# Kernel tuning notes

Hardware: AMD Instinct MI355X
Metric: run time of the kernel (lower is better)

## Reference

```python
import jax, jax.numpy as jnp
import numpy as np


def mish(x):
    return x * jnp.tanh(jax.nn.softplus(x))


def gcn(x, W, b, src, dst):
    # PyG GCNConv: h = D^-1/2 (A+I) D^-1/2 (x W) + b, aggregation at dst=edge_index[1]
    n = x.shape[0]
    h = x @ W
    deg = jax.ops.segment_sum(jnp.ones(src.shape[0], x.dtype), dst, num_segments=n) + 1.0
    dinv = jax.lax.rsqrt(deg)
    msg = h[src] * (dinv[src] * dinv[dst])[:, None]
    agg = jax.ops.segment_sum(msg, dst, num_segments=n)
    return agg + h * (dinv * dinv)[:, None] + b


def pool_mean(x, seg, num_segments):
    s = jax.ops.segment_sum(x, seg, num_segments=num_segments)
    c = jax.ops.segment_sum(jnp.ones(x.shape[0], x.dtype), seg, num_segments=num_segments)
    return s / jnp.maximum(c, 1.0)[:, None]


def attention(x, qW, qb, kW, kb, vW, vb, G):
    # x: [G*R, in_feats] -> per-graph self-attention over ROIs (dropout is identity in eval)
    R = x.shape[0] // G
    xc = x.reshape(G, R, x.shape[1])
    Q = xc @ qW + qb
    K = xc @ kW + kb
    Vv = xc @ vW + vb
    scores = jnp.einsum('gqd,gkd->gqk', Q, K) / (Q.shape[-1] ** 0.5)
    w = jax.nn.softmax(scores, axis=-1)
    out = jnp.einsum('gqk,gkd->gqd', w, Vv).reshape(G * R, Vv.shape[-1])
    return out, w.mean(axis=0)


def closs(a, b, temp=0.6):
    a = a / jnp.maximum(jnp.linalg.norm(a, axis=1, keepdims=True), 1e-12)
    b = b / jnp.maximum(jnp.linalg.norm(b, axis=1, keepdims=True), 1e-12)
    logits = (a @ b.T) / temp
    return -jnp.mean(jnp.diagonal(jax.nn.log_softmax(logits, axis=1)))


def setup_inputs() -> dict:
    key = jax.random.key(0)
    G, R1, R2, F_IN, H, OUT, DEG, V = 512, 200, 160, 128, 64, 64, 16, 64
    N1, N2 = G * R1, G * R2
    ks = iter(jax.random.split(key, 64))
    d = {}
    d['x1'] = jax.random.normal(next(ks), (N1, R1 + 3), jnp.float32)
    d['x2'] = jax.random.normal(next(ks), (N2, R2 + 3), jnp.float32)

    def lin(name, i, o):
        d[name + '_W'] = jax.random.normal(next(ks), (i, o), jnp.float32) * (i ** -0.5)
        d[name + '_b'] = jnp.zeros((o,), jnp.float32)

    lin('fcl', R1 + 3, F_IN); lin('fcr', R2 + 3, F_IN)
    lin('fcl1', R1, F_IN); lin('fcr1', R2, F_IN)
    lin('a1_q', F_IN, OUT); lin('a1_k', F_IN, OUT); lin('a1_v', F_IN, OUT)
    lin('a2_q', F_IN, OUT); lin('a2_k', F_IN, OUT); lin('a2_v', F_IN, OUT)
    lin('conv', F_IN, H); lin('conv1', H, H)
    lin('mlp', H, OUT)
    lin('fc1a', OUT * 4, F_IN); lin('fc1b', F_IN, 2)

    def edges(k, R):
        k1, k2 = jax.random.split(k)
        off = (jnp.arange(G, dtype=jnp.int32) * R)[:, None]
        src = jax.random.randint(k1, (G, R * DEG), 0, R, jnp.int32) + off
        dst = jax.random.randint(k2, (G, R * DEG), 0, R, jnp.int32) + off
        return jnp.stack([src.reshape(-1), dst.reshape(-1)])

    d['edge_index1'] = edges(next(ks), R1)
    d['edge_index2'] = edges(next(ks), R2)
    d['batch1'] = jnp.repeat(jnp.arange(G, dtype=jnp.int32), R1)
    d['batch2'] = jnp.repeat(jnp.arange(G, dtype=jnp.int32), R2)

    def sub(k, R):
        # one visited-node set (as in RW_subgraph) tiled per graph with offsets
        vis = jnp.sort(jax.random.permutation(k, R)[:V]).astype(jnp.int32)
        return (vis[None, :] + (jnp.arange(G, dtype=jnp.int32) * R)[:, None]).reshape(-1)

    d['sub_idx1'] = sub(next(ks), R1)
    d['sub_idx2'] = sub(next(ks), R2)
    d['num_graphs'] = G
    return d


def reference(x1, x2, fcl_W, fcl_b, fcr_W, fcr_b, fcl1_W, fcl1_b, fcr1_W, fcr1_b,
              a1_q_W, a1_q_b, a1_k_W, a1_k_b, a1_v_W, a1_v_b,
              a2_q_W, a2_q_b, a2_k_W, a2_k_b, a2_v_W, a2_v_b,
              conv_W, conv_b, conv1_W, conv1_b, mlp_W, mlp_b,
              fc1a_W, fc1a_b, fc1b_W, fc1b_b,
              edge_index1, edge_index2, batch1, batch2, sub_idx1, sub_idx2, num_graphs):
    G = int(num_graphs)
    src1, dst1 = edge_index1[0], edge_index1[1]
    src2, dst2 = edge_index2[0], edge_index2[1]

    z1 = x1[:, :-3] @ fcl1_W + fcl1_b
    z2 = x2[:, :-3] @ fcr1_W + fcr1_b
    z1, aw1 = attention(z1, a1_q_W, a1_q_b, a1_k_W, a1_k_b, a1_v_W, a1_v_b, G)
    z2, aw2 = attention(z2, a2_q_W, a2_q_b, a2_k_W, a2_k_b, a2_v_W, a2_v_b, G)
    z1 = pool_mean(z1, batch1, G)
    z2 = pool_mean(z2, batch2, G)

    h1 = x1 @ fcl_W + fcl_b
    h2 = x2 @ fcr_W + fcr_b
    o1 = mish(gcn(h1, conv_W, conv_b, src1, dst1))
    o2 = mish(gcn(h2, conv_W, conv_b, src2, dst2))
    o1 = gcn(o1, conv1_W, conv1_b, src1, dst1)
    o2 = gcn(o2, conv1_W, conv1_b, src2, dst2)

    s1 = o1[sub_idx1] @ mlp_W + mlp_b
    s2 = o2[sub_idx2] @ mlp_W + mlp_b
    s1 = pool_mean(s1, batch1[sub_idx1], G)
    s2 = pool_mean(s2, batch2[sub_idx2], G)

    c_loss = closs(s1, z2) + closs(z1, s2)
    feat = jnp.concatenate([s1, z1, s2, z2], axis=1)
    out = mish(feat @ fc1a_W + fc1a_b) @ fc1b_W + fc1b_b
    return c_loss, out, aw1, aw2
```

## Files before the change

kernel.cpp:

```cpp
#include <hip/hip_runtime.h>
#include <math.h>

#define TPB 256
#define MAXEP 4608

typedef float f32x4 __attribute__((ext_vector_type(4)));
typedef __bf16 bfv8 __attribute__((ext_vector_type(8)));

union U8 { uint4 q; unsigned short us[8]; __bf16 b[8]; bfv8 v; };

__device__ __forceinline__ unsigned short f2bfu(float f) {
  union { __bf16 h; unsigned short u; } x;
  x.h = (__bf16)f;
  return x.u;
}
__device__ __forceinline__ float bfu2f(unsigned short u) {
  return __uint_as_float((unsigned)u << 16);
}

__device__ __forceinline__ float mish_f(float x) {
  float sp = fmaxf(x, 0.f) + log1pf(expf(-fabsf(x)));
  return x * tanhf(sp);
}

__device__ __forceinline__ U8 loadA_f32(const float* Af, int kb, int K, bool rowok) {
  U8 u;
  if (rowok && kb + 8 <= K) {
    float4 f0 = *(const float4*)(Af + kb);
    float4 f1 = *(const float4*)(Af + kb + 4);
    u.b[0]=(__bf16)f0.x; u.b[1]=(__bf16)f0.y; u.b[2]=(__bf16)f0.z; u.b[3]=(__bf16)f0.w;
    u.b[4]=(__bf16)f1.x; u.b[5]=(__bf16)f1.y; u.b[6]=(__bf16)f1.z; u.b[7]=(__bf16)f1.w;
  } else {
#pragma unroll
    for (int j = 0; j < 8; ++j) {
      float f = (rowok && kb + j < K) ? Af[kb + j] : 0.f;
      u.b[j] = (__bf16)f;
    }
  }
  return u;
}

template<bool ABF16, bool CBF16, bool MISH, int NJ, int KPMAX>
__global__ __launch_bounds__(256) void gemm2(
    const void* __restrict__ Av, const unsigned short* __restrict__ Bt,
    const float* __restrict__ bias, void* __restrict__ Cv,
    int N, int M, int K, int lda, int ldc,
    long sA, long sB, long sC, float alpha, int Kpad)
{
  constexpr int BM = NJ * 16;
  __shared__ unsigned short Bs[BM * KPMAX];

  const int tid = threadIdx.x;
  const int col0 = blockIdx.x * BM, row0 = blockIdx.y * 64;

  {
    const unsigned short* Bp = Bt + (long)blockIdx.z * sB + (long)col0 * Kpad;
    int rows = M - col0; if (rows > BM) rows = BM;
    const int total = rows * Kpad;
    for (int i = tid * 8; i < total; i += TPB * 32) {
      uint4 a0, a1, a2, a3;
      bool b1 = i + TPB * 8  < total;
      bool b2 = i + TPB * 16 < total;
      bool b3 = i + TPB * 24 < total;
      a0 = *(const uint4*)&Bp[i];
      if (b1) a1 = *(const uint4*)&Bp[i + TPB * 8];
      if (b2) a2 = *(const uint4*)&Bp[i + TPB * 16];
      if (b3) a3 = *(const uint4*)&Bp[i + TPB * 24];
      *(uint4*)&Bs[i] = a0;
      if (b1) *(uint4*)&Bs[i + TPB * 8]  = a1;
      if (b2) *(uint4*)&Bs[i + TPB * 16] = a2;
      if (b3) *(uint4*)&Bs[i + TPB * 24] = a3;
    }
  }

  const int lane = tid & 63, w = tid >> 6;
  const int mrow = lane & 15, kg = lane >> 4;
  const int arow = row0 + w * 16 + mrow;
  const bool rowok = arow < N;

  const unsigned short* Ah = nullptr;
  const float* Af = nullptr;
  if (ABF16) Ah = (const unsigned short*)Av + (long)blockIdx.z * sA + (long)arow * lda;
  else       Af = (const float*)Av + (long)blockIdx.z * sA + (long)arow * lda;

  U8 ua;
  if (ABF16) ua.q = *(const uint4*)(Ah + kg * 8);
  else       ua   = loadA_f32(Af, kg * 8, K, rowok);

  __syncthreads();

  f32x4 acc[NJ];
#pragma unroll
  for (int j = 0; j < NJ; ++j) acc[j] = (f32x4)0.f;

  for (int k0 = 0; k0 < K; k0 += 32) {
    U8 un;
    bool more = (k0 + 32) < K;
    if (more) {
      if (ABF16) un.q = *(const uint4*)(Ah + k0 + 32 + kg * 8);
      else       un   = loadA_f32(Af, k0 + 32 + kg * 8, K, rowok);
    }
    const int kb = k0 + kg * 8;
#pragma unroll
    for (int j = 0; j < NJ; ++j) {
      U8 ub;
      ub.q = *(const uint4*)&Bs[(j * 16 + mrow) * Kpad + kb];
      acc[j] = __builtin_amdgcn_mfma_f32_16x16x32_bf16(ua.v, ub.v, acc[j], 0, 0, 0);
    }
    if (more) ua = un;
  }

  long cbase = (long)blockIdx.z * sC;
#pragma unroll
  for (int j = 0; j < NJ; ++j) {
    int gc = col0 + j * 16 + mrow;
    if (gc >= M) continue;
    float bb = bias ? bias[gc] : 0.f;
#pragma unroll
    for (int r = 0; r < 4; ++r) {
      int gr = row0 + w * 16 + kg * 4 + r;
      if (gr >= N) continue;
      float v = acc[j][r] * alpha + bb;
      if (MISH) v = mish_f(v);
      if (CBF16) ((unsigned short*)Cv)[cbase + (long)gr * ldc + gc] = f2bfu(v);
      else       ((float*)Cv)[cbase + (long)gr * ldc + gc] = v;
    }
  }
}

static inline int kpad_of(int K) { return ((K + 31) / 32) * 32 + 8; }

struct PrepSeg { const float* src; void* dst; int K, M, Kpad, kind; };
struct PrepArgs { PrepSeg s[19]; };

__global__ __launch_bounds__(256) void prep_weights(PrepArgs a) {
  PrepSeg sg = a.s[blockIdx.x];
  if (sg.kind == 0) {
    unsigned short* d = (unsigned short*)sg.dst;
    int tot = sg.M * sg.Kpad;
    for (int i = threadIdx.x; i < tot; i += TPB) {
      int m = i / sg.Kpad, k = i - m * sg.Kpad;
      float f = (k < sg.K) ? sg.src[(long)k * sg.M + m] : 0.f;
      d[i] = f2bfu(f);
    }
  } else {
    float* d = (float*)sg.dst;
    for (int i = threadIdx.x; i < sg.K; i += TPB) d[i] = sg.src[i];
  }
}

__global__ __launch_bounds__(256) void ktvt2(
    const unsigned short* __restrict__ QKV, unsigned short* __restrict__ Kt,
    unsigned short* __restrict__ Vt, int R, int Rpad)
{
  __shared__ unsigned short tile[64][72];
  int g = blockIdx.x, tid = threadIdx.x;
  const unsigned short* q = QKV + (long)g * R * 192;
  unsigned short* kt = Kt + (long)g * R * 72;
  unsigned short* vt = Vt + (long)g * 64 * Rpad;

  {
    int c = tid & 63, w = tid >> 6;
    for (int r = w; r < R; r += 4)
      kt[r * 72 + c] = q[(long)r * 192 + 64 + c];
  }

  for (int r0 = 0; r0 < Rpad; r0 += 64) {
    __syncthreads();
    for (int i = tid; i < 64 * 64; i += TPB) {
      int rr = i >> 6, cc = i & 63;
      int r = r0 + rr;
      tile[cc][rr] = (r < R) ? q[(long)r * 192 + 128 + cc] : (unsigned short)0;
    }
    __syncthreads();
    int c = tid >> 2, j0 = (tid & 3) * 16;
    int lim = Rpad - r0; if (lim > 64) lim = 64;
    for (int jj = j0; jj < j0 + 16 && jj < lim; jj += 8) {
      uint4 qv = *(const uint4*)&tile[c][jj];
      *(uint4*)&vt[(long)c * Rpad + r0 + jj] = qv;
    }
  }
}

__global__ __launch_bounds__(256) void adj_build(
    const int* __restrict__ src, const int* __restrict__ dst,
    unsigned short* __restrict__ Adj, int R, int Rpad, int EPG)
{
  __shared__ float dinv_s[256];
  __shared__ unsigned short ssrc[MAXEP];
  __shared__ int cnt[256];
  __shared__ int scan[256];
  __shared__ int offx[257];
  __shared__ int cur[256];
  __shared__ float rowbuf[4][256];

  int g = blockIdx.x, tid = threadIdx.x;
  long ebase = (long)g * EPG;
  int gR = g * R;

  cnt[tid] = 0;
  __syncthreads();
  for (int e = tid; e < EPG; e += TPB)
    atomicAdd(&cnt[dst[ebase + e] - gR], 1);
  __syncthreads();

  int x = cnt[tid];
  int pc = (x + 7) & ~7;
  scan[tid] = pc;
  __syncthreads();
#pragma unroll
  for (int s = 1; s < 256; s <<= 1) {
    int t = (tid >= s) ? scan[tid - s] : 0;
    __syncthreads();
    scan[tid] += t;
    __syncthreads();
  }
  if (tid == 0) offx[0] = 0;
  offx[tid + 1] = scan[tid];
  cur[tid] = scan[tid] - pc;
  dinv_s[tid] = rsqrtf((float)x + 1.f);
  {
    unsigned dummy2 = 0xFFFFFFFFu;
    for (int i = tid; i < MAXEP / 2; i += TPB) ((unsigned*)ssrc)[i] = dummy2;
  }
  __syncthreads();

  for (int e = tid; e < EPG; e += TPB) {
    int d = dst[ebase + e] - gR;
    int s = src[ebase + e] - gR;
    int pos = atomicAdd(&cur[d], 1);
    ssrc[pos] = (unsigned short)s;
  }
  __syncthreads();

  int lane = tid & 63, w = tid >> 6;
  float* rb = rowbuf[w];
  for (int d = w; d < R; d += 4) {
#pragma unroll
    for (int i = 0; i < 4; ++i) rb[lane + i * 64] = 0.f;
    int i0 = offx[d], i1 = offx[d + 1];
    for (int i = i0 + lane; i < i1; i += 64) {
      int s = ssrc[i];
      if (s < R) atomicAdd(&rb[s], dinv_s[s]);
    }
    float dd = dinv_s[d];
    int c0 = lane * 4;
    if (c0 < Rpad) {
      ushort4 o;
      float v0 = rb[c0]     + (c0     == d ? dd : 0.f);
      float v1 = rb[c0 + 1] + (c0 + 1 == d ? dd : 0.f);
      float v2 = rb[c0 + 2] + (c0 + 2 == d ? dd : 0.f);
      float v3 = rb[c0 + 3] + (c0 + 3 == d ? dd : 0.f);
      o.x = f2bfu(v0 * dd); o.y = f2bfu(v1 * dd);
      o.z = f2bfu(v2 * dd); o.w = f2bfu(v3 * dd);
      *(ushort4*)&Adj[((long)gR + d) * Rpad + c0] = o;
    }
  }
}

__global__ __launch_bounds__(256) void transp64(
    const unsigned short* __restrict__ X, unsigned short* __restrict__ XT,
    int R, int Rpad)
{
  __shared__ unsigned short tile[64][72];
  int g = blockIdx.x, tid = threadIdx.x;
  const unsigned short* xg = X + (long)g * R * 64;
  unsigned short* xt = XT + (long)g * 64 * Rpad;
  for (int r0 = 0; r0 < Rpad; r0 += 64) {
    __syncthreads();
    for (int i = tid; i < 64 * 64; i += TPB) {
      int rr = i >> 6, cc = i & 63;
      int r = r0 + rr;
      tile[cc][rr] = (r < R) ? xg[(long)r * 64 + cc] : (unsigned short)0;
    }
    __syncthreads();
    int c = tid >> 2, j0 = (tid & 3) * 16;
    int lim = Rpad - r0; if (lim > 64) lim = 64;
    for (int jj = j0; jj < j0 + 16 && jj < lim; jj += 8) {
      uint4 q = *(const uint4*)&tile[c][jj];
      *(uint4*)&xt[(long)c * Rpad + r0 + jj] = q;
    }
  }
}

__global__ __launch_bounds__(256) void softmax_bf16(unsigned short* __restrict__ S,
                                                    int R, long rows)
{
  long wid = (long)blockIdx.x * 4 + (threadIdx.x >> 6);
  if (wid >= rows) return;
  int lane = threadIdx.x & 63;
  unsigned short* row = S + wid * R;
  float v[4];
  float mx = -1e30f;
#pragma unroll
  for (int t = 0; t < 4; ++t) {
    int j = lane + t * 64;
    v[t] = (j < R) ? bfu2f(row[j]) : -1e30f;
    mx = fmaxf(mx, v[t]);
  }
#pragma unroll
  for (int o = 32; o; o >>= 1) mx = fmaxf(mx, __shfl_xor(mx, o));
  float s = 0.f;
#pragma unroll
  for (int t = 0; t < 4; ++t) {
    int j = lane + t * 64;
    if (j < R) { v[t] = expf(v[t] - mx); s += v[t]; }
  }
#pragma unroll
  for (int o = 32; o; o >>= 1) s += __shfl_xor(s, o);
  float inv = 1.f / s;
#pragma unroll
  for (int t = 0; t < 4; ++t) {
    int j = lane + t * 64;
    if (j < R) row[j] = f2bfu(v[t] * inv);
  }
}

__global__ void meang_bf16(const unsigned short* __restrict__ S, float* __restrict__ out,
                           int RR, int G, float inv)
{
  int idx = blockIdx.x * TPB + threadIdx.x;
  if (idx >= RR) return;
  const unsigned short* p = S + idx;
  float s = 0.f;
  for (int g = 0; g + 8 <= G; g += 8) {
    s += bfu2f(p[(long)g * RR])       + bfu2f(p[(long)(g + 1) * RR]) +
         bfu2f(p[(long)(g + 2) * RR]) + bfu2f(p[(long)(g + 3) * RR]) +
         bfu2f(p[(long)(g + 4) * RR]) + bfu2f(p[(long)(g + 5) * RR]) +
         bfu2f(p[(long)(g + 6) * RR]) + bfu2f(p[(long)(g + 7) * RR]);
  }
  out[idx] = s * inv;
}

__global__ __launch_bounds__(256) void pool_mean_bf16(const unsigned short* __restrict__ X,
                                                      float* __restrict__ out, int R)
{
  __shared__ float part[4][64];
  int g = blockIdx.x, lane = threadIdx.x & 63, w = threadIdx.x >> 6;
  float s = 0.f;
  for (int r = w; r < R; r += 4)
    s += bfu2f(X[((long)g * R + r) * 64 + lane]);
  part[w][lane] = s;
  __syncthreads();
  if (w == 0)
    out[g * 64 + lane] = (part[0][lane] + part[1][lane] + part[2][lane] + part[3][lane]) * (1.f / R);
}

__global__ __launch_bounds__(64) void sub_mean_kernel(const unsigned short* __restrict__ X,
                                                      const int* __restrict__ sub,
                                                      float* __restrict__ out, int V)
{
  int g = blockIdx.x, lane = threadIdx.x;
  float s = 0.f;
  for (int v = 0; v + 4 <= V; v += 4) {
    int i0 = sub[g * V + v],     i1 = sub[g * V + v + 1];
    int i2 = sub[g * V + v + 2], i3 = sub[g * V + v + 3];
    s += bfu2f(X[(long)i0 * 64 + lane]) + bfu2f(X[(long)i1 * 64 + lane]) +
         bfu2f(X[(long)i2 * 64 + lane]) + bfu2f(X[(long)i3 * 64 + lane]);
  }
  out[g * 64 + lane] = s * (1.f / V);
}

__global__ __launch_bounds__(64) void norm_rows_kernel(const float* __restrict__ X,
                                                       float* __restrict__ Y)
{
  int g = blockIdx.x, lane = threadIdx.x;
  float x = X[g * 64 + lane];
  float ss = x * x;
#pragma unroll
  for (int o = 32; o; o >>= 1) ss += __shfl_xor(ss, o);
  float n = fmaxf(sqrtf(ss), 1e-12f);
  Y[g * 64 + lane] = x / n;
}

__global__ __launch_bounds__(256) void closs_kernel(const float* __restrict__ An,
                                                    const float* __restrict__ Bn,
                                                    float* __restrict__ loss, int G,
                                                    float invTemp, float coef)
{
  int i = blockIdx.x;
  __shared__ float arow[64];
  __shared__ float logits[512];
  __shared__ float red[256];
  int t = threadIdx.x;
  if (t < 64) arow[t] = An[i * 64 + t];
  __syncthreads();
  for (int j = t; j < G; j += 256) {
    const float* bp = Bn + (long)j * 64;
    float d = 0.f;
#pragma unroll
    for (int k = 0; k < 64; ++k) d = fmaf(arow[k], bp[k], d);
    logits[j] = d * invTemp;
  }
  __syncthreads();
  float mx = -1e30f;
  for (int j = t; j < G; j += 256) mx = fmaxf(mx, logits[j]);
  red[t] = mx; __syncthreads();
  for (int o = 128; o; o >>= 1) { if (t < o) red[t] = fmaxf(red[t], red[t + o]); __syncthreads(); }
  mx = red[0]; __syncthreads();
  float s = 0.f;
  for (int j = t; j < G; j += 256) s += expf(logits[j] - mx);
  red[t] = s; __syncthreads();
  for (int o = 128; o; o >>= 1) { if (t < o) red[t] += red[t + o]; __syncthreads(); }
  if (t == 0) {
    float lse = mx + logf(red[0]);
    atomicAdd(loss, coef * (lse - logits[i]));
  }
}

__global__ __launch_bounds__(128) void head_kernel(
    const float* __restrict__ s1, const float* __restrict__ z1,
    const float* __restrict__ s2, const float* __restrict__ z2,
    const float* __restrict__ W1, const float* __restrict__ b1,
    const float* __restrict__ W2, const float* __restrict__ b2,
    float* __restrict__ out)
{
  int g = blockIdx.x, t = threadIdx.x;
  __shared__ float feat[256];
  __shared__ float hid[128];
  if (t < 64) {
    feat[t]       = s1[g * 64 + t];
    feat[64 + t]  = z1[g * 64 + t];
    feat[128 + t] = s2[g * 64 + t];
    feat[192 + t] = z2[g * 64 + t];
  }
  __syncthreads();
  float acc = b1[t];
  for (int k = 0; k < 256; ++k) acc = fmaf(feat[k], W1[k * 128 + t], acc);
  hid[t] = mish_f(acc);
  __syncthreads();
  if (t < 2) {
    float a2 = b2[t];
#pragma unroll
    for (int k = 0; k < 128; ++k) a2 = fmaf(hid[k], W2[k * 2 + t], a2);
    out[g * 2 + t] = a2;
  }
}

#define LAUNCH_GEMM(ABF,CBF,MISH,NJ,KP, A,B,BI,C, N,M,K,LDA,LDC,SA,SB,SC,BAT,AL,KPAD) \
  { dim3 g_(((M)+(NJ)*16-1)/((NJ)*16), ((N)+63)/64, (BAT)); \
    gemm2<ABF,CBF,MISH,NJ,KP><<<g_,256,0,stream>>>((A),(B),(BI),(C),(N),(M),(K),(LDA),(LDC),(SA),(SB),(SC),(AL),(KPAD)); }

extern "C" void kernel_launch(void* const* d_in, const int* in_sizes, int n_in,
                              void* d_out, int out_size, void* d_ws, size_t ws_size,
                              hipStream_t stream)
{
  const float* x1     = (const float*)d_in[0];
  const float* x2     = (const float*)d_in[1];
  const float* fcl_W  = (const float*)d_in[2];  const float* fcl_b  = (const float*)d_in[3];
  const float* fcr_W  = (const float*)d_in[4];  const float* fcr_b  = (const float*)d_in[5];
  const float* fcl1_W = (const float*)d_in[6];  const float* fcl1_b = (const float*)d_in[7];
  const float* fcr1_W = (const float*)d_in[8];  const float* fcr1_b = (const float*)d_in[9];
  const float* a1qW = (const float*)d_in[10]; const float* a1qb = (const float*)d_in[11];
  const float* a1kW = (const float*)d_in[12]; const float* a1kb = (const float*)d_in[13];
  const float* a1vW = (const float*)d_in[14]; const float* a1vb = (const float*)d_in[15];
  const float* a2qW = (const float*)d_in[16]; const float* a2qb = (const float*)d_in[17];
  const float* a2kW = (const float*)d_in[18]; const float* a2kb = (const float*)d_in[19];
  const float* a2vW = (const float*)d_in[20]; const float* a2vb = (const float*)d_in[21];
  const float* convW  = (const float*)d_in[22]; const float* convb  = (const float*)d_in[23];
  const float* conv1W = (const float*)d_in[24]; const float* conv1b = (const float*)d_in[25];
  const float* mlpW   = (const float*)d_in[26]; const float* mlpb   = (const float*)d_in[27];
  const float* fc1aW  = (const float*)d_in[28]; const float* fc1ab  = (const float*)d_in[29];
  const float* fc1bW  = (const float*)d_in[30]; const float* fc1bb  = (const float*)d_in[31];
  const int* ei1  = (const int*)d_in[32];
  const int* ei2  = (const int*)d_in[33];
  const int* sub1 = (const int*)d_in[36];
  const int* sub2 = (const int*)d_in[37];

  const int R1 = in_sizes[6] / 128;
  const int R2 = in_sizes[8] / 128;
  const int N1 = in_sizes[34];
  const int N2 = in_sizes[35];
  const int G  = N1 / R1;
  const int E1 = in_sizes[32] / 2, E2 = in_sizes[33] / 2;
  const int EPG1 = E1 / G, EPG2 = E2 / G;
  const int V = in_sizes[36] / G;

  const int Kp1  = kpad_of(R1);
  const int Kp2  = kpad_of(R2);
  const int Kp1f = kpad_of(R1 + 3);
  const int Kp2f = kpad_of(R2 + 3);
  const int Rpad1 = Kp1, Rpad2 = Kp2;

  char* wp = (char*)d_ws;
  auto alloc = [&](size_t bytes) -> char* {
    char* p = wp; wp += (bytes + 255) & ~(size_t)255; return p;
  };
  size_t raSh = (size_t)G * R1 * R1;
  if ((size_t)N1 * 128 > raSh) raSh = (size_t)N1 * 128;
  unsigned short* RA = (unsigned short*)alloc(raSh * 2);
  unsigned short* RB = (unsigned short*)alloc((size_t)N1 * 192 * 2);
  unsigned short* Kt = (unsigned short*)alloc((size_t)G * R1 * 72 * 2);
  unsigned short* Vt = (unsigned short*)alloc((size_t)G * 64 * Rpad1 * 2);
  unsigned short* W5 = (unsigned short*)alloc((size_t)N1 * 64 * 2);
  unsigned short* Adj1 = (unsigned short*)alloc((size_t)G * R1 * Rpad1 * 2);
  unsigned short* Adj2 = (unsigned short*)alloc((size_t)G * R2 * Rpad2 * 2);
  unsigned short* fcl1t  = (unsigned short*)alloc((size_t)128 * Kp1 * 2);
  unsigned short* fcr1t  = (unsigned short*)alloc((size_t)128 * Kp2 * 2);
  unsigned short* fclt   = (unsigned short*)alloc((size_t)128 * Kp1f * 2);
  unsigned short* fcrt   = (unsigned short*)alloc((size_t)128 * Kp2f * 2);
  unsigned short* Wc1t   = (unsigned short*)alloc((size_t)192 * 136 * 2);
  unsigned short* Wc2t   = (unsigned short*)alloc((size_t)192 * 136 * 2);
  unsigned short* convt  = (unsigned short*)alloc((size_t)64 * 136 * 2);
  unsigned short* conv1t = (unsigned short*)alloc((size_t)64 * 72 * 2);
  unsigned short* mlpt   = (unsigned short*)alloc((size_t)64 * 72 * 2);
  float* bc1 = (float*)alloc(192 * 4);
  float* bc2 = (float*)alloc(192 * 4);
  float* Pz1 = (float*)alloc((size_t)G * 64 * 4);
  float* Pz2 = (float*)alloc((size_t)G * 64 * 4);
  float* Ps1 = (float*)alloc((size_t)G * 64 * 4);
  float* Ps2 = (float*)alloc((size_t)G * 64 * 4);
  float* Mt  = (float*)alloc((size_t)G * 64 * 4);
  float* n_s1 = (float*)alloc((size_t)G * 64 * 4);
  float* n_z2 = (float*)alloc((size_t)G * 64 * 4);
  float* n_z1 = (float*)alloc((size_t)G * 64 * 4);
  float* n_s2 = (float*)alloc((size_t)G * 64 * 4);
  (void)alloc(65536);

  float* loss = (float*)d_out;
  float* outp = loss + 1;
  float* aw1  = outp + (size_t)G * 2;
  float* aw2  = aw1 + (size_t)R1 * R1;

  hipMemsetAsync(d_out, 0, sizeof(float), stream);

  PrepArgs pa;
  int seg = 0;
  auto addp = [&](const float* s, unsigned short* d, int K, int M, int Kp) {
    pa.s[seg].src = s; pa.s[seg].dst = d; pa.s[seg].K = K; pa.s[seg].M = M;
    pa.s[seg].Kpad = Kp; pa.s[seg].kind = 0; seg++;
  };
  auto addb = [&](const float* s, float* d, int n) {
    pa.s[seg].src = s; pa.s[seg].dst = d; pa.s[seg].K = n; pa.s[seg].M = 0;
    pa.s[seg].Kpad = 0; pa.s[seg].kind = 1; seg++;
  };
  addp(fcl1_W, fcl1t, R1, 128, Kp1);
  addp(fcr1_W, fcr1t, R2, 128, Kp2);
  addp(fcl_W,  fclt,  R1 + 3, 128, Kp1f);
  addp(fcr_W,  fcrt,  R2 + 3, 128, Kp2f);
  addp(a1qW, Wc1t,             128, 64, 136);
  addp(a1kW, Wc1t + 64 * 136,  128, 64, 136);
  addp(a1vW, Wc1t + 128 * 136, 128, 64, 136);
  addp(a2qW, Wc2t,             128, 64, 136);
  addp(a2kW, Wc2t + 64 * 136,  128, 64, 136);
  addp(a2vW, Wc2t + 128 * 136, 128, 64, 136);
  addp(convW,  convt,  128, 64, 136);
  addp(conv1W, conv1t, 64, 64, 72);
  addp(mlpW,   mlpt,   64, 64, 72);
  addb(a1qb, bc1, 64); addb(a1kb, bc1 + 64, 64); addb(a1vb, bc1 + 128, 64);
  addb(a2qb, bc2, 64); addb(a2kb, bc2 + 64, 64); addb(a2vb, bc2 + 128, 64);
  prep_weights<<<seg, 256, 0, stream>>>(pa);

  LAUNCH_GEMM(false, true, false, 8, 232, x1, fcl1t, fcl1_b, RA,
              N1, 128, R1, R1 + 3, 128, 0, 0, 0, 1, 1.f, Kp1);
  LAUNCH_GEMM(true, true, false, 12, 136, RA, Wc1t, bc1, RB,
              N1, 192, 128, 128, 192, 0, 0, 0, 1, 1.f, 136);
  ktvt2<<<G, 256, 0, stream>>>(RB, Kt, Vt, R1, Rpad1);
  LAUNCH_GEMM(true, true, false, 8, 72, RB, Kt, nullptr, RA,
              R1, R1, 64, 192, R1, (long)R1 * 192, (long)R1 * 72, (long)R1 * R1,
              G, 0.125f, 72);
  {
    long rows = (long)G * R1;
    softmax_bf16<<<(int)((rows + 3) / 4), 256, 0, stream>>>(RA, R1, rows);
    meang_bf16<<<(R1 * R1 + TPB - 1) / TPB, TPB, 0, stream>>>(RA, aw1, R1 * R1, G, 1.f / G);
  }
  LAUNCH_GEMM(true, true, false, 4, 232, RA, Vt, nullptr, W5,
              R1, 64, R1, R1, 64, (long)R1 * R1, (long)64 * Rpad1, (long)R1 * 64,
              G, 1.f, Rpad1);
  pool_mean_bf16<<<G, 256, 0, stream>>>(W5, Pz1, R1);

  LAUNCH_GEMM(false, true, false, 8, 232, x2, fcr1t, fcr1_b, RA,
              N2, 128, R2, R2 + 3, 128, 0, 0, 0, 1, 1.f, Kp2);
  LAUNCH_GEMM(true, true, false, 12, 136, RA, Wc2t, bc2, RB,
              N2, 192, 128, 128, 192, 0, 0, 0, 1, 1.f, 136);
  ktvt2<<<G, 256, 0, stream>>>(RB, Kt, Vt, R2, Rpad2);
  LAUNCH_GEMM(true, true, false, 8, 72, RB, Kt, nullptr, RA,
              R2, R2, 64, 192, R2, (long)R2 * 192, (long)R2 * 72, (long)R2 * R2,
              G, 0.125f, 72);
  {
    long rows = (long)G * R2;
    softmax_bf16<<<(int)((rows + 3) / 4), 256, 0, stream>>>(RA, R2, rows);
    meang_bf16<<<(R2 * R2 + TPB - 1) / TPB, TPB, 0, stream>>>(RA, aw2, R2 * R2, G, 1.f / G);
  }
  LAUNCH_GEMM(true, true, false, 4, 232, RA, Vt, nullptr, W5,
              R2, 64, R2, R2, 64, (long)R2 * R2, (long)64 * Rpad2, (long)R2 * 64,
              G, 1.f, Rpad2);
  pool_mean_bf16<<<G, 256, 0, stream>>>(W5, Pz2, R2);

  unsigned short* hW0 = RB;
  unsigned short* hW1 = RB + (size_t)N1 * 64;
  unsigned short* hW2 = RB + (size_t)N1 * 128;
  LAUNCH_GEMM(false, true, false, 8, 232, x1, fclt, fcl_b, RA,
              N1, 128, R1 + 3, R1 + 3, 128, 0, 0, 0, 1, 1.f, Kp1f);
  LAUNCH_GEMM(true, true, false, 4, 136, RA, convt, nullptr, hW0,
              N1, 64, 128, 128, 64, 0, 0, 0, 1, 1.f, 136);
  adj_build<<<G, 256, 0, stream>>>(ei1, ei1 + E1, Adj1, R1, Rpad1, EPG1);
  transp64<<<G, 256, 0, stream>>>(hW0, Vt, R1, Rpad1);
  LAUNCH_GEMM(true, true, true, 4, 232, Adj1, Vt, convb, hW1,
              R1, 64, R1, Rpad1, 64, (long)R1 * Rpad1, (long)64 * Rpad1, (long)R1 * 64,
              G, 1.f, Rpad1);
  LAUNCH_GEMM(true, true, false, 4, 136, hW1, conv1t, nullptr, hW2,
              N1, 64, 64, 64, 64, 0, 0, 0, 1, 1.f, 72);
  transp64<<<G, 256, 0, stream>>>(hW2, Vt, R1, Rpad1);
  LAUNCH_GEMM(true, true, false, 4, 232, Adj1, Vt, conv1b, hW0,
              R1, 64, R1, Rpad1, 64, (long)R1 * Rpad1, (long)64 * Rpad1, (long)R1 * 64,
              G, 1.f, Rpad1);
  sub_mean_kernel<<<G, 64, 0, stream>>>(hW0, sub1, Mt, V);
  LAUNCH_GEMM(false, false, false, 4, 136, Mt, mlpt, mlpb, Ps1,
              G, 64, 64, 64, 64, 0, 0, 0, 1, 1.f, 72);

  LAUNCH_GEMM(false, true, false, 8, 232, x2, fcrt, fcr_b, RA,
              N2, 128, R2 + 3, R2 + 3, 128, 0, 0, 0, 1, 1.f, Kp2f);
  LAUNCH_GEMM(true, true, false, 4, 136, RA, convt, nullptr, hW0,
              N2, 64, 128, 128, 64, 0, 0, 0, 1, 1.f, 136);
  adj_build<<<G, 256, 0, stream>>>(ei2, ei2 + E2, Adj2, R2, Rpad2, EPG2);
  transp64<<<G, 256, 0, stream>>>(hW0, Vt, R2, Rpad2);
  LAUNCH_GEMM(true, true, true, 4, 232, Adj2, Vt, convb, hW1,
              R2, 64, R2, Rpad2, 64, (long)R2 * Rpad2, (long)64 * Rpad2, (long)R2 * 64,
              G, 1.f, Rpad2);
  LAUNCH_GEMM(true, true, false, 4, 136, hW1, conv1t, nullptr, hW2,
              N2, 64, 64, 64, 64, 0, 0, 0, 1, 1.f, 72);
  transp64<<<G, 256, 0, stream>>>(hW2, Vt, R2, Rpad2);
  LAUNCH_GEMM(true, true, false, 4, 232, Adj2, Vt, conv1b, hW0,
              R2, 64, R2, Rpad2, 64, (long)R2 * Rpad2, (long)64 * Rpad2, (long)R2 * 64,
              G, 1.f, Rpad2);
  sub_mean_kernel<<<G, 64, 0, stream>>>(hW0, sub2, Mt, V);
  LAUNCH_GEMM(false, false, false, 4, 136, Mt, mlpt, mlpb, Ps2,
              G, 64, 64, 64, 64, 0, 0, 0, 1, 1.f, 72);

  norm_rows_kernel<<<G, 64, 0, stream>>>(Ps1, n_s1);
  norm_rows_kernel<<<G, 64, 0, stream>>>(Pz2, n_z2);
  norm_rows_kernel<<<G, 64, 0, stream>>>(Pz1, n_z1);
  norm_rows_kernel<<<G, 64, 0, stream>>>(Ps2, n_s2);
  const float invTemp = 1.f / 0.6f;
  closs_kernel<<<G, 256, 0, stream>>>(n_s1, n_z2, loss, G, invTemp, 1.f / G);
  closs_kernel<<<G, 256, 0, stream>>>(n_z1, n_s2, loss, G, invTemp, 1.f / G);

  head_kernel<<<G, 128, 0, stream>>>(Ps1, Pz1, Ps2, Pz2, fc1aW, fc1ab, fc1bW, fc1bb, outp);
}
```

Baseline: 960.8 us.

## Fold consecutive linear layers into combined weights before the big GEMMs

Precomputes the products fcl1·Wqkv, fcr1·Wqkv, fcl·conv and fcr·conv (with combined biases) per call, so each of the four large input projections becomes a single GEMM straight from x instead of two chained GEMMs with an intermediate 128-wide activation. This removes the intermediate write and read and the second GEMM launch, trading them for small per-call weight-combination GEMMs and bias kernels. Because the combined weights are rounded to bf16 once rather than rounding the intermediate activation, numerics shift slightly.

```diff
diff --git a/kernel.cpp b/kernel.cpp
--- a/kernel.cpp
+++ b/kernel.cpp
@@ -143,10 +143,30 @@
       float f = (k < sg.K) ? sg.src[(long)k * sg.M + m] : 0.f;
       d[i] = f2bfu(f);
     }
-  } else {
+  } else if (sg.kind == 1) {
     float* d = (float*)sg.dst;
     for (int i = threadIdx.x; i < sg.K; i += TPB) d[i] = sg.src[i];
-  }
+  } else {
+    unsigned short* d = (unsigned short*)sg.dst;
+    int tot = sg.M * sg.Kpad;
+    for (int i = threadIdx.x; i < tot; i += TPB) {
+      int m = i / sg.Kpad, k = i - m * sg.Kpad;
+      float f = (k < sg.K) ? sg.src[(long)m * sg.K + k] : 0.f;
+      d[i] = f2bfu(f);
+    }
+  }
+}
+
+__global__ __launch_bounds__(64) void bias_comb(const float* __restrict__ b_in,
+                                                const unsigned short* __restrict__ Wt,
+                                                int ldw, const float* __restrict__ bc,
+                                                float* __restrict__ out, int M, int K)
+{
+  int m = blockIdx.x * 64 + threadIdx.x;
+  if (m >= M) return;
+  float s = bc ? bc[m] : 0.f;
+  for (int k = 0; k < K; ++k) s += b_in[k] * bfu2f(Wt[(long)m * ldw + k]);
+  out[m] = s;
 }
 
 __global__ __launch_bounds__(256) void ktvt2(
@@ -495,17 +515,28 @@
   unsigned short* W5 = (unsigned short*)alloc((size_t)N1 * 64 * 2);
   unsigned short* Adj1 = (unsigned short*)alloc((size_t)G * R1 * Rpad1 * 2);
   unsigned short* Adj2 = (unsigned short*)alloc((size_t)G * R2 * Rpad2 * 2);
-  unsigned short* fcl1t  = (unsigned short*)alloc((size_t)128 * Kp1 * 2);
-  unsigned short* fcr1t  = (unsigned short*)alloc((size_t)128 * Kp2 * 2);
-  unsigned short* fclt   = (unsigned short*)alloc((size_t)128 * Kp1f * 2);
-  unsigned short* fcrt   = (unsigned short*)alloc((size_t)128 * Kp2f * 2);
+  unsigned short* fcl1n = (unsigned short*)alloc((size_t)R1 * 136 * 2);
+  unsigned short* fcr1n = (unsigned short*)alloc((size_t)R2 * 136 * 2);
+  unsigned short* fcln  = (unsigned short*)alloc((size_t)(R1 + 3) * 136 * 2);
+  unsigned short* fcrn  = (unsigned short*)alloc((size_t)(R2 + 3) * 136 * 2);
   unsigned short* Wc1t   = (unsigned short*)alloc((size_t)192 * 136 * 2);
   unsigned short* Wc2t   = (unsigned short*)alloc((size_t)192 * 136 * 2);
   unsigned short* convt  = (unsigned short*)alloc((size_t)64 * 136 * 2);
   unsigned short* conv1t = (unsigned short*)alloc((size_t)64 * 72 * 2);
   unsigned short* mlpt   = (unsigned short*)alloc((size_t)64 * 72 * 2);
+  size_t wzB1 = (size_t)192 * Kp1 * 2, wzB2 = (size_t)192 * Kp2 * 2;
+  size_t wgB1 = (size_t)64 * Kp1f * 2, wgB2 = (size_t)64 * Kp2f * 2;
+  char* comb = alloc(wzB1 + wzB2 + wgB1 + wgB2);
+  unsigned short* Wz1t = (unsigned short*)comb;
+  unsigned short* Wz2t = (unsigned short*)(comb + wzB1);
+  unsigned short* Wg1t = (unsigned short*)(comb + wzB1 + wzB2);
+  unsigned short* Wg2t = (unsigned short*)(comb + wzB1 + wzB2 + wgB1);
   float* bc1 = (float*)alloc(192 * 4);
   float* bc2 = (float*)alloc(192 * 4);
+  float* bz1 = (float*)alloc(192 * 4);
+  float* bz2 = (float*)alloc(192 * 4);
+  float* bg1 = (float*)alloc(64 * 4);
+  float* bg2 = (float*)alloc(64 * 4);
   float* Pz1 = (float*)alloc((size_t)G * 64 * 4);
   float* Pz2 = (float*)alloc((size_t)G * 64 * 4);
   float* Ps1 = (float*)alloc((size_t)G * 64 * 4);
@@ -523,38 +554,50 @@
   float* aw2  = aw1 + (size_t)R1 * R1;
 
   hipMemsetAsync(d_out, 0, sizeof(float), stream);
+  hipMemsetAsync(comb, 0, wzB1 + wzB2 + wgB1 + wgB2, stream);
 
   PrepArgs pa;
   int seg = 0;
-  auto addp = [&](const float* s, unsigned short* d, int K, int M, int Kp) {
+  auto addp = [&](const float* s, unsigned short* d, int K, int M, int Kp, int kind) {
     pa.s[seg].src = s; pa.s[seg].dst = d; pa.s[seg].K = K; pa.s[seg].M = M;
-    pa.s[seg].Kpad = Kp; pa.s[seg].kind = 0; seg++;
+    pa.s[seg].Kpad = Kp; pa.s[seg].kind = kind; seg++;
   };
   auto addb = [&](const float* s, float* d, int n) {
     pa.s[seg].src = s; pa.s[seg].dst = d; pa.s[seg].K = n; pa.s[seg].M = 0;
     pa.s[seg].Kpad = 0; pa.s[seg].kind = 1; seg++;
   };
-  addp(fcl1_W, fcl1t, R1, 128, Kp1);
-  addp(fcr1_W, fcr1t, R2, 128, Kp2);
-  addp(fcl_W,  fclt,  R1 + 3, 128, Kp1f);
-  addp(fcr_W,  fcrt,  R2 + 3, 128, Kp2f);
-  addp(a1qW, Wc1t,             128, 64, 136);
-  addp(a1kW, Wc1t + 64 * 136,  128, 64, 136);
-  addp(a1vW, Wc1t + 128 * 136, 128, 64, 136);
-  addp(a2qW, Wc2t,             128, 64, 136);
-  addp(a2kW, Wc2t + 64 * 136,  128, 64, 136);
-  addp(a2vW, Wc2t + 128 * 136, 128, 64, 136);
-  addp(convW,  convt,  128, 64, 136);
-  addp(conv1W, conv1t, 64, 64, 72);
-  addp(mlpW,   mlpt,   64, 64, 72);
+  addp(fcl1_W, fcl1n, 128, R1, 136, 2);
+  addp(fcr1_W, fcr1n, 128, R2, 136, 2);
+  addp(fcl_W,  fcln,  128, R1 + 3, 136, 2);
+  addp(fcr_W,  fcrn,  128, R2 + 3, 136, 2);
+  addp(a1qW, Wc1t,             128, 64, 136, 0);
+  addp(a1kW, Wc1t + 64 * 136,  128, 64, 136, 0);
+  addp(a1vW, Wc1t + 128 * 136, 128, 64, 136, 0);
+  addp(a2qW, Wc2t,             128, 64, 136, 0);
+  addp(a2kW, Wc2t + 64 * 136,  128, 64, 136, 0);
+  addp(a2vW, Wc2t + 128 * 136, 128, 64, 136, 0);
+  addp(convW,  convt,  128, 64, 136, 0);
+  addp(conv1W, conv1t, 64, 64, 72, 0);
+  addp(mlpW,   mlpt,   64, 64, 72, 0);
   addb(a1qb, bc1, 64); addb(a1kb, bc1 + 64, 64); addb(a1vb, bc1 + 128, 64);
   addb(a2qb, bc2, 64); addb(a2kb, bc2 + 64, 64); addb(a2vb, bc2 + 128, 64);
   prep_weights<<<seg, 256, 0, stream>>>(pa);
 
-  LAUNCH_GEMM(false, true, false, 8, 232, x1, fcl1t, fcl1_b, RA,
-              N1, 128, R1, R1 + 3, 128, 0, 0, 0, 1, 1.f, Kp1);
-  LAUNCH_GEMM(true, true, false, 12, 136, RA, Wc1t, bc1, RB,
-              N1, 192, 128, 128, 192, 0, 0, 0, 1, 1.f, 136);
+  LAUNCH_GEMM(true, true, false, 8, 136, Wc1t, fcl1n, nullptr, Wz1t,
+              192, R1, 128, 136, Kp1, 0, 0, 0, 1, 1.f, 136);
+  LAUNCH_GEMM(true, true, false, 8, 136, Wc2t, fcr1n, nullptr, Wz2t,
+              192, R2, 128, 136, Kp2, 0, 0, 0, 1, 1.f, 136);
+  LAUNCH_GEMM(true, true, false, 8, 136, convt, fcln, nullptr, Wg1t,
+              64, R1 + 3, 128, 136, Kp1f, 0, 0, 0, 1, 1.f, 136);
+  LAUNCH_GEMM(true, true, false, 8, 136, convt, fcrn, nullptr, Wg2t,
+              64, R2 + 3, 128, 136, Kp2f, 0, 0, 0, 1, 1.f, 136);
+  bias_comb<<<3, 64, 0, stream>>>(fcl1_b, Wc1t, 136, bc1, bz1, 192, 128);
+  bias_comb<<<3, 64, 0, stream>>>(fcr1_b, Wc2t, 136, bc2, bz2, 192, 128);
+  bias_comb<<<1, 64, 0, stream>>>(fcl_b, convt, 136, nullptr, bg1, 64, 128);
+  bias_comb<<<1, 64, 0, stream>>>(fcr_b, convt, 136, nullptr, bg2, 64, 128);
+
+  LAUNCH_GEMM(false, true, false, 6, 232, x1, Wz1t, bz1, RB,
+              N1, 192, R1, R1 + 3, 192, 0, 0, 0, 1, 1.f, Kp1);
   ktvt2<<<G, 256, 0, stream>>>(RB, Kt, Vt, R1, Rpad1);
   LAUNCH_GEMM(true, true, false, 8, 72, RB, Kt, nullptr, RA,
               R1, R1, 64, 192, R1, (long)R1 * 192, (long)R1 * 72, (long)R1 * R1,
@@ -569,10 +612,8 @@
               G, 1.f, Rpad1);
   pool_mean_bf16<<<G, 256, 0, stream>>>(W5, Pz1, R1);
 
-  LAUNCH_GEMM(false, true, false, 8, 232, x2, fcr1t, fcr1_b, RA,
-              N2, 128, R2, R2 + 3, 128, 0, 0, 0, 1, 1.f, Kp2);
-  LAUNCH_GEMM(true, true, false, 12, 136, RA, Wc2t, bc2, RB,
-              N2, 192, 128, 128, 192, 0, 0, 0, 1, 1.f, 136);
+  LAUNCH_GEMM(false, true, false, 6, 232, x2, Wz2t, bz2, RB,
+              N2, 192, R2, R2 + 3, 192, 0, 0, 0, 1, 1.f, Kp2);
   ktvt2<<<G, 256, 0, stream>>>(RB, Kt, Vt, R2, Rpad2);
   LAUNCH_GEMM(true, true, false, 8, 72, RB, Kt, nullptr, RA,
               R2, R2, 64, 192, R2, (long)R2 * 192, (long)R2 * 72, (long)R2 * R2,
@@ -590,10 +631,8 @@
   unsigned short* hW0 = RB;
   unsigned short* hW1 = RB + (size_t)N1 * 64;
   unsigned short* hW2 = RB + (size_t)N1 * 128;
-  LAUNCH_GEMM(false, true, false, 8, 232, x1, fclt, fcl_b, RA,
-              N1, 128, R1 + 3, R1 + 3, 128, 0, 0, 0, 1, 1.f, Kp1f);
-  LAUNCH_GEMM(true, true, false, 4, 136, RA, convt, nullptr, hW0,
-              N1, 64, 128, 128, 64, 0, 0, 0, 1, 1.f, 136);
+  LAUNCH_GEMM(false, true, false, 4, 232, x1, Wg1t, bg1, hW0,
+              N1, 64, R1 + 3, R1 + 3, 64, 0, 0, 0, 1, 1.f, Kp1f);
   adj_build<<<G, 256, 0, stream>>>(ei1, ei1 + E1, Adj1, R1, Rpad1, EPG1);
   transp64<<<G, 256, 0, stream>>>(hW0, Vt, R1, Rpad1);
   LAUNCH_GEMM(true, true, true, 4, 232, Adj1, Vt, convb, hW1,
@@ -609,10 +648,8 @@
   LAUNCH_GEMM(false, false, false, 4, 136, Mt, mlpt, mlpb, Ps1,
               G, 64, 64, 64, 64, 0, 0, 0, 1, 1.f, 72);
 
-  LAUNCH_GEMM(false, true, false, 8, 232, x2, fcrt, fcr_b, RA,
-              N2, 128, R2 + 3, R2 + 3, 128, 0, 0, 0, 1, 1.f, Kp2f);
-  LAUNCH_GEMM(true, true, false, 4, 136, RA, convt, nullptr, hW0,
-              N2, 64, 128, 128, 64, 0, 0, 0, 1, 1.f, 136);
+  LAUNCH_GEMM(false, true, false, 4, 232, x2, Wg2t, bg2, hW0,
+              N2, 64, R2 + 3, R2 + 3, 64, 0, 0, 0, 1, 1.f, Kp2f);
   adj_build<<<G, 256, 0, stream>>>(ei2, ei2 + E2, Adj2, R2, Rpad2, EPG2);
   transp64<<<G, 256, 0, stream>>>(hW0, Vt, R2, Rpad2);
   LAUNCH_GEMM(true, true, true, 4, 232, Adj2, Vt, convb, hW1,
```

New measurement: 953.0 us. No clear change (-0.8%).
